# Performance work log

Measured on AMD Instinct MI355X. Metric: run time of the kernel, lower is better.

## Reference

```python
import jax, jax.numpy as jnp
from jax import lax
import numpy as np

NUM_HEADS = 4
EPS = 1e-5


def refl_conv(x, W, stride):
    # ReflectionPad2d(1) + Conv2d(k=3, bias=False), NCHW/OIHW
    x = jnp.pad(x, ((0, 0), (0, 0), (1, 1), (1, 1)), mode='reflect')
    return lax.conv_general_dilated(x, W, (stride, stride), 'VALID',
                                    dimension_numbers=('NCHW', 'OIHW', 'NCHW'))


def instance_norm(x):
    # nn.InstanceNorm2d (affine=False, biased var, eps=1e-5)
    m = jnp.mean(x, axis=(2, 3), keepdims=True)
    v = jnp.var(x, axis=(2, 3), keepdims=True)
    return (x - m) * lax.rsqrt(v + EPS)


def iln(x, rho, gamma, beta):
    # UGATIT Instance-Layer Norm; torch.var default is unbiased (ddof=1)
    in_m = jnp.mean(x, axis=(2, 3), keepdims=True)
    in_v = jnp.var(x, axis=(2, 3), keepdims=True, ddof=1)
    ln_m = jnp.mean(x, axis=(1, 2, 3), keepdims=True)
    ln_v = jnp.var(x, axis=(1, 2, 3), keepdims=True, ddof=1)
    out = rho * (x - in_m) * lax.rsqrt(in_v + EPS) \
        + (1.0 - rho) * (x - ln_m) * lax.rsqrt(ln_v + EPS)
    return out * gamma + beta


def upsample2(x):
    # nn.Upsample(scale_factor=2, mode='nearest')
    return jnp.repeat(jnp.repeat(x, 2, axis=2), 2, axis=3)


def pos_encoding(x):
    # sin/cos positional encoding over flattened HW, added per channel
    b, c, h, w = x.shape
    half = c // 2
    pos = jnp.arange(h * w, dtype=x.dtype)                  # [L]
    depths = jnp.arange(half, dtype=x.dtype) / half          # [c/2]
    rates = 1.0 / (10000.0 ** depths)
    ang = pos[:, None] * rates[None, :]                      # [L, c/2]
    pe = jnp.concatenate([jnp.sin(ang), jnp.cos(ang)], axis=-1)  # [L, c]
    return (x.reshape(b, c, h * w) + pe.T[None]).reshape(b, c, h, w)


def mha(q, k, v, num_heads):
    # q,k,v: [b, n, c]; hand-rolled QK^T-softmax-V (dropout=0)
    b, n, c = q.shape
    d = c // num_heads
    split = lambda t: t.reshape(b, t.shape[1], num_heads, d).transpose(0, 2, 1, 3)
    qh, kh, vh = split(q), split(k), split(v)                # [b, h, n, d]
    scores = jnp.einsum('bhid,bhjd->bhij', qh, kh) * (d ** -0.5)
    attn = jax.nn.softmax(scores, axis=-1)                   # full NxN materialized
    out = jnp.einsum('bhij,bhjd->bhid', attn, vh)
    return out.transpose(0, 2, 1, 3).reshape(b, n, c)


def setup_inputs() -> dict:
    key = jax.random.key(0)
    ks = jax.random.split(key, 8)
    W = 0.05
    return {
        'y': jax.random.normal(ks[0], (2, 256, 64, 64), jnp.float32),
        's': jax.random.normal(ks[1], (2, 128, 128, 128), jnp.float32),
        'w_blue_s': jax.random.normal(ks[2], (128, 128, 3, 3), jnp.float32) * W,
        'w_blue_y': jax.random.normal(ks[3], (128, 256, 3, 3), jnp.float32) * W,
        'w_purple': jax.random.normal(ks[4], (128, 128, 3, 3), jnp.float32) * W,
        'rho_p': jax.random.uniform(ks[5], (1, 128, 1, 1), jnp.float32),
        'gamma_p': jnp.ones((1, 128, 1, 1), jnp.float32),
        'beta_p': jnp.zeros((1, 128, 1, 1), jnp.float32),
        'w_green': jax.random.normal(ks[6], (128, 256, 3, 3), jnp.float32) * W,
        'rho_g': jax.random.uniform(ks[7], (1, 128, 1, 1), jnp.float32),
        'gamma_g': jnp.ones((1, 128, 1, 1), jnp.float32),
        'beta_g': jnp.zeros((1, 128, 1, 1), jnp.float32),
    }


def reference(y, s, w_blue_s, w_blue_y, w_purple, rho_p, gamma_p, beta_p,
              w_green, rho_g, gamma_g, beta_g):
    b, yc, yh, yw = y.shape
    sc = yc // 2
    # green_y: upsample -> refl conv -> ILN -> SiLU
    up_y = jax.nn.silu(iln(refl_conv(upsample2(y), w_green, 1), rho_g, gamma_g, beta_g))
    y_pe = pos_encoding(y)
    s_pe = pos_encoding(s)
    # blue_y (stride 1) -> q = k; blue_s (stride 2) -> v
    q2d = jax.nn.silu(instance_norm(refl_conv(y_pe, w_blue_y, 1)))   # [b, sc, yh, yw]
    v2d = jax.nn.silu(instance_norm(refl_conv(s_pe, w_blue_s, 2)))   # [b, sc, yh, yw]
    q = q2d.reshape(b, sc, yh * yw).transpose(0, 2, 1)               # [b, N, sc]
    v = v2d.reshape(b, sc, -1).transpose(0, 2, 1)
    out = mha(q, q, v, NUM_HEADS)                                     # [b, N, sc]
    mha2d = out.transpose(0, 2, 1).reshape(b, sc, yh, yw)
    # purple: upsample -> refl conv -> ILN -> sigmoid; gate s
    z = jax.nn.sigmoid(iln(refl_conv(upsample2(mha2d), w_purple, 1),
                           rho_p, gamma_p, beta_p)) * s
    return jnp.concatenate([z, up_y], axis=1)                         # [b, yc, 2yh, 2yw]
```

## Files before the change

kernel.cpp:

```cpp
#include <hip/hip_runtime.h>
#include <math.h>

#define EPS 1e-5f

typedef __attribute__((ext_vector_type(8))) _Float16 f16x8;
typedef __attribute__((ext_vector_type(4))) float f32x4;
typedef __attribute__((ext_vector_type(2))) __fp16 fp16x2;

union H8u { ushort4 u[2]; uint4 q; f16x8 h; };
union PKu { fp16x2 h; unsigned int u; };

__device__ __forceinline__ float sigmoidf_(float x){ return 1.f/(1.f+__expf(-x)); }

__device__ __forceinline__ unsigned short f2h(float f){
  union { _Float16 h; unsigned short u; } c;
  c.h = (_Float16)f;
  return c.u;
}

__device__ __forceinline__ void block_reduce2(float& s, float& s2){
  __shared__ float ls[16], ls2[16];
  #pragma unroll
  for (int off = 32; off; off >>= 1){
    s  += __shfl_down(s, off);
    s2 += __shfl_down(s2, off);
  }
  int wid = threadIdx.x >> 6, lane = threadIdx.x & 63;
  int nw = blockDim.x >> 6;
  if (lane == 0){ ls[wid] = s; ls2[wid] = s2; }
  __syncthreads();
  if (threadIdx.x == 0){
    float a = ls[0], b = ls2[0];
    for (int i = 1; i < nw; i++){ a += ls[i]; b += ls2[i]; }
    ls[0] = a; ls2[0] = b;
  }
  __syncthreads();
  s = ls[0]; s2 = ls2[0];
}

__device__ __forceinline__ unsigned short wffP_elem(const float* __restrict__ w, int Cin, int idx){
  int NCH = Cin >> 5;
  int per_tap = NCH << 9;
  int e = idx & 7, lane = (idx >> 3) & 63, chunk = (idx >> 9) % NCH;
  int tap = (idx / per_tap) % 9, coB = idx / (9 * per_tap);
  int lg = lane >> 4, lr = lane & 15;
  int co = coB * 16 + lr;
  int ch = chunk * 32 + ((e < 4) ? lg * 4 + e : 16 + lg * 4 + e - 4);
  return f2h(w[((long)co * Cin + ch) * 9 + tap]);
}

__device__ __forceinline__ unsigned short wffF_elem(const float* __restrict__ w, int Cin, int idx){
  int NCH = Cin >> 5;
  int per_tap = NCH << 9;
  int per_p = 8 * 4 * per_tap;
  int e = idx & 7, lane = (idx >> 3) & 63, chunk = (idx >> 9) % NCH;
  int tap = (idx / per_tap) % 4;
  int coB = (idx / (4 * per_tap)) % 8;
  int p = idx / per_p;
  int ph = p >> 1, pw = p & 1, kr = tap >> 1, kc = tap & 1;
  int lg = lane >> 4, lr = lane & 15;
  int co = coB * 16 + lr;
  int ch = chunk * 32 + ((e < 4) ? lg * 4 + e : 16 + lg * 4 + e - 4);
  const float* wb = &w[((long)co * Cin + ch) * 9];
  float sum = 0.f;
  for (int kh = 0; kh < 3; kh++){
    bool rok = (ph == 0) ? (kr == 0 ? kh == 0 : kh >= 1)
                         : (kr == 0 ? kh <= 1 : kh == 2);
    if (!rok) continue;
    for (int kw = 0; kw < 3; kw++){
      bool cok = (pw == 0) ? (kc == 0 ? kw == 0 : kw >= 1)
                           : (kc == 0 ? kw <= 1 : kw == 2);
      if (cok) sum += wb[kh * 3 + kw];
    }
  }
  return f2h(sum);
}

__global__ __launch_bounds__(256) void prep_all_kernel(
    const float* __restrict__ y, const float* __restrict__ s,
    unsigned short* __restrict__ y_peT, unsigned short* __restrict__ yT,
    unsigned short* __restrict__ s_peT,
    const float* __restrict__ wby, const float* __restrict__ wbs,
    const float* __restrict__ wg,  const float* __restrict__ wp,
    unsigned short* __restrict__ oby, unsigned short* __restrict__ obs,
    unsigned short* __restrict__ og,  unsigned short* __restrict__ op){
  __shared__ unsigned short tile[64][72];
  __shared__ unsigned short tile2[64][72];
  int bid = blockIdx.x;
  int tid = threadIdx.x;
  if (bid >= 1536){
    const int T0 = 294912, T1 = T0 + 147456, T2 = T1 + 524288, T3 = T2 + 262144;
    for (int idx = (bid - 1536) * 256 + tid; idx < T3; idx += 300 * 256){
      if (idx < T0)       oby[idx]      = wffP_elem(wby, 256, idx);
      else if (idx < T1)  obs[idx - T0] = wffP_elem(wbs, 128, idx - T0);
      else if (idx < T2)  og[idx - T1]  = wffF_elem(wg, 256, idx - T1);
      else                op[idx - T2]  = wffF_elem(wp, 128, idx - T2);
    }
    return;
  }
  const float* x; unsigned short *xt, *xt2;
  int C, L, half, bx, by, bz;
  if (bid < 512){
    x = y; xt = y_peT; xt2 = yT; C = 256; L = 4096; half = 128;
    bx = bid & 63; by = (bid >> 6) & 3; bz = bid >> 8;
  } else {
    int b2 = bid - 512;
    x = s; xt = s_peT; xt2 = nullptr; C = 128; L = 16384; half = 64;
    bx = b2 & 255; by = (b2 >> 8) & 1; bz = b2 >> 9;
  }
  int c0 = by * 64, l0 = bx * 64;
  int b = bz;
  const float l2r = 13.28771237954945f;
  #pragma unroll
  for (int i = 0; i < 4; i++){
    int id = tid + i * 256;
    int c = id >> 4, ch = (id & 15) * 4;
    int cg = c0 + c;
    float4 v = *(const float4*)&x[((long)b * C + cg) * L + l0 + ch];
    int d = cg < half ? cg : cg - half;
    float rate = exp2f(-l2r * (float)d / (float)half);
    float a0 = (float)(l0 + ch) * rate;
    float pe0, pe1, pe2, pe3;
    if (cg < half){ pe0 = sinf(a0); pe1 = sinf(a0 + rate); pe2 = sinf(a0 + 2.f*rate); pe3 = sinf(a0 + 3.f*rate); }
    else          { pe0 = cosf(a0); pe1 = cosf(a0 + rate); pe2 = cosf(a0 + 2.f*rate); pe3 = cosf(a0 + 3.f*rate); }
    ushort4 o;
    o.x = f2h(v.x + pe0); o.y = f2h(v.y + pe1);
    o.z = f2h(v.z + pe2); o.w = f2h(v.w + pe3);
    *(ushort4*)&tile[c][ch] = o;
    if (xt2){
      ushort4 o2;
      o2.x = f2h(v.x); o2.y = f2h(v.y); o2.z = f2h(v.z); o2.w = f2h(v.w);
      *(ushort4*)&tile2[c][ch] = o2;
    }
  }
  __syncthreads();
  #pragma unroll
  for (int i = 0; i < 2; i++){
    int id = tid + i * 256;
    int l = id >> 3, ch = (id & 7) * 8;
    ushort4 a, bq;
    a.x = tile[ch+0][l]; a.y = tile[ch+1][l]; a.z = tile[ch+2][l]; a.w = tile[ch+3][l];
    bq.x = tile[ch+4][l]; bq.y = tile[ch+5][l]; bq.z = tile[ch+6][l]; bq.w = tile[ch+7][l];
    unsigned short* opt = &xt[((long)b * L + l0 + l) * C + c0 + ch];
    *(ushort4*)opt = a;
    *(ushort4*)(opt + 4) = bq;
    if (xt2){
      ushort4 a2, b2;
      a2.x = tile2[ch+0][l]; a2.y = tile2[ch+1][l]; a2.z = tile2[ch+2][l]; a2.w = tile2[ch+3][l];
      b2.x = tile2[ch+4][l]; b2.y = tile2[ch+5][l]; b2.z = tile2[ch+6][l]; b2.w = tile2[ch+7][l];
      unsigned short* op2 = &xt2[((long)b * L + l0 + l) * C + c0 + ch];
      *(ushort4*)op2 = a2;
      *(ushort4*)(op2 + 4) = b2;
    }
  }
}

template<int NTAP, int CSHIFT, int UP, int STATS>
__device__ __forceinline__ void conv_body(
    const unsigned short* __restrict__ xt, const unsigned short* __restrict__ wff,
    unsigned short* __restrict__ out,
    float* __restrict__ psum, float* __restrict__ psq, int which,
    int Hin, int Win, int stride, int Wout, int woutLog, int HWout,
    int bz, char* stage, int* rowIdx){
  constexpr int Cin = 8 << CSHIFT;
  constexpr int NCHUNK = 1 << (CSHIFT - 2);
  int tid = threadIdx.x;
  int lane = tid & 63, wid = tid >> 6;
  int lg = lane >> 4, lr = lane & 15;
  int b, par = 0;
  if (UP){ par = bz & 3; b = bz >> 2; } else b = bz;
  const unsigned short* xb = xt + (long)b * Hin * Win * Cin;
  int coB = blockIdx.y * 4 + wid;

  if (UP){
    int ph = par >> 1, pw = par & 1;
    int ii = blockIdx.x;
    int VH = 2 * Hin, VW = 2 * Win;
    for (int id = tid; id < NTAP * 64; id += 256){
      int tap = id >> 6, r = id & 63;
      int kr = tap >> 1, kc = tap & 1;
      int v = 2 * ii + (ph == 0 ? (kr == 0 ? -1 : 0) : (kr == 0 ? 0 : 2));
      v = v < 0 ? -v : (v >= VH ? 2 * VH - 2 - v : v);
      int u = 2 * r + (pw == 0 ? (kc == 0 ? -1 : 0) : (kc == 0 ? 0 : 2));
      u = u < 0 ? -u : (u >= VW ? 2 * VW - 2 - u : u);
      rowIdx[tap * 64 + r] = (v >> 1) * Win + (u >> 1);
    }
  } else {
    int sp0 = blockIdx.x * 64;
    for (int id = tid; id < NTAP * 64; id += 256){
      int tap = id >> 6, r = id & 63;
      int kh = tap / 3, kw = tap - kh * 3;
      int sp = sp0 + r;
      int oh = sp >> woutLog, ow = sp & (Wout - 1);
      int ih = oh * stride - 1 + kh;
      ih = ih < 0 ? -ih : (ih >= Hin ? 2 * Hin - 2 - ih : ih);
      int iw = ow * stride - 1 + kw;
      iw = iw < 0 ? -iw : (iw >= Win ? 2 * Win - 2 - iw : iw);
      rowIdx[tap * 64 + r] = ih * Win + iw;
    }
  }

  f32x4 acc[4];
  #pragma unroll
  for (int f = 0; f < 4; f++) acc[f] = (f32x4){0.f, 0.f, 0.f, 0.f};

  const unsigned short* wbase =
      wff + ((long)((UP ? par : 0) * 8 + coB) * NTAP) * (NCHUNK * 512) + lane * 8;

  for (int tap = 0; tap < NTAP; tap++){
    __syncthreads();
    #pragma unroll
    for (int i2 = 0; i2 < NCHUNK; i2++){
      int id = tid + (i2 << 8);
      int sp = id >> CSHIFT;
      int c8 = (id & ((1 << CSHIFT) - 1)) << 3;
      int chunk = c8 >> 5, c = c8 & 31;
      int lgb = (c & 15) >> 2, hoff = (c >> 4) & 1;
      uint4 g = *(const uint4*)&xb[(long)rowIdx[tap * 64 + sp] * Cin + c8];
      int slot = ((chunk * 4 + (sp >> 4)) * 64 + lgb * 16 + (sp & 15)) * 16
                 + hoff * 8 + chunk * 16;
      *(uint2*)(stage + slot)       = make_uint2(g.x, g.y);
      *(uint2*)(stage + slot + 256) = make_uint2(g.z, g.w);
    }
    __syncthreads();
    const unsigned short* wp = wbase + (long)tap * (NCHUNK * 512);
    #pragma unroll
    for (int ch = 0; ch < NCHUNK; ch++){
      H8u A; A.q = *(const uint4*)(wp + ch * 512);
      #pragma unroll
      for (int f = 0; f < 4; f++){
        H8u X; X.q = *(const uint4*)(stage + ((ch * 4 + f) * 64 + lane) * 16 + ch * 16);
        acc[f] = __builtin_amdgcn_mfma_f32_16x16x32_f16(A.h, X.h, acc[f], 0, 0, 0);
      }
    }
  }

  unsigned short* ob = out + (long)b * 128 * HWout;
  #pragma unroll
  for (int f = 0; f < 4; f++){
    int spl = f * 16 + lr;
    long opos;
    if (UP){
      int oh = 2 * blockIdx.x + (par >> 1);
      int ow = 2 * spl + (par & 1);
      opos = (long)oh * Wout + ow;
    } else opos = (long)blockIdx.x * 64 + spl;
    #pragma unroll
    for (int r = 0; r < 4; r++){
      int co = coB * 16 + lg * 4 + r;
      ob[(long)co * HWout + opos] = f2h(acc[f][r]);
    }
  }

  if constexpr (STATS){
    float ts[4], tq[4];
    #pragma unroll
    for (int r = 0; r < 4; r++){ ts[r] = 0.f; tq[r] = 0.f; }
    #pragma unroll
    for (int f = 0; f < 4; f++)
      #pragma unroll
      for (int r = 0; r < 4; r++){
        float hv = (float)(_Float16)acc[f][r];
        ts[r] += hv; tq[r] += hv * hv;
      }
    #pragma unroll
    for (int off = 1; off < 16; off <<= 1){
      #pragma unroll
      for (int r = 0; r < 4; r++){
        ts[r] += __shfl_xor(ts[r], off);
        tq[r] += __shfl_xor(tq[r], off);
      }
    }
    if (lr == 0){
      int strip = blockIdx.x * 4 + par;
      #pragma unroll
      for (int r = 0; r < 4; r++){
        int co = coB * 16 + lg * 4 + r;
        long pidx = (((long)which * 2 + b) * 128 + co) * 256 + strip;
        psum[pidx] = ts[r];
        psq[pidx]  = tq[r];
      }
    }
  }
}

__global__ __launch_bounds__(256) void conv_blue_kernel(
    const unsigned short* __restrict__ y_peT, const unsigned short* __restrict__ s_peT,
    const unsigned short* __restrict__ wby, const unsigned short* __restrict__ wbs,
    unsigned short* __restrict__ qbuf, unsigned short* __restrict__ vbuf){
  __shared__ __align__(16) char stage[8 * 4112];
  __shared__ int rowIdx[9 * 64];
  int z = blockIdx.z;
  if (z < 2)
    conv_body<9,5,0,0>(y_peT, wby, qbuf, nullptr, nullptr, 0,
                       64, 64, 1, 64, 6, 4096, z, stage, rowIdx);
  else
    conv_body<9,4,0,0>(s_peT, wbs, vbuf, nullptr, nullptr, 0,
                       128, 128, 2, 64, 6, 4096, z - 2, stage, rowIdx);
}

__global__ __launch_bounds__(256) void conv_up_kernel(
    const unsigned short* __restrict__ yT, const unsigned short* __restrict__ mhaT,
    const unsigned short* __restrict__ wg, const unsigned short* __restrict__ wp,
    unsigned short* __restrict__ green_h, unsigned short* __restrict__ purple_h,
    float* __restrict__ psum, float* __restrict__ psq){
  __shared__ __align__(16) char stage[8 * 4112];
  __shared__ int rowIdx[4 * 64];
  int z = blockIdx.z;
  if (z < 8)
    conv_body<4,5,1,1>(yT, wg, green_h, psum, psq, 0,
                       64, 64, 1, 128, 7, 16384, z, stage, rowIdx);
  else
    conv_body<4,4,1,1>(mhaT, wp, purple_h, psum, psq, 1,
                       64, 64, 1, 128, 7, 16384, z - 8, stage, rowIdx);
}

__global__ __launch_bounds__(256) void in_silu2_kernel(
    const unsigned short* __restrict__ qx, unsigned short* __restrict__ outT,
    const unsigned short* __restrict__ vx, unsigned short* __restrict__ outV, int HW){
  int which = blockIdx.y;
  int bc = blockIdx.x;
  const unsigned short* p = (which ? vx : qx) + (long)bc * HW;
  int i0 = threadIdx.x * 16;
  H8u a, b2;
  a.q  = *(const uint4*)&p[i0];
  b2.q = *(const uint4*)&p[i0 + 8];
  float v[16];
  float s = 0.f, s2 = 0.f;
  #pragma unroll
  for (int j = 0; j < 8; j++){ v[j] = (float)a.h[j]; v[8+j] = (float)b2.h[j]; }
  #pragma unroll
  for (int j = 0; j < 16; j++){ s += v[j]; s2 += v[j]*v[j]; }
  block_reduce2(s, s2);
  float mean = s / (float)HW;
  float var  = s2 / (float)HW - mean * mean;
  float rstd = rsqrtf(var + EPS);
  if (which == 0){
    int b = bc >> 7, cg = bc & 127, h = cg >> 5, d = cg & 31;
    unsigned short* op = outT + ((long)(b * 4 + h) * HW) * 32 + d;
    #pragma unroll
    for (int j = 0; j < 16; j++){
      float t = (v[j] - mean) * rstd;
      t = t * sigmoidf_(t);
      op[(long)(i0 + j) * 32] = f2h(t);
    }
  } else {
    H8u o0, o1;
    #pragma unroll
    for (int j = 0; j < 8; j++){
      float t = (v[j] - mean) * rstd;
      o0.h[j] = (_Float16)(t * sigmoidf_(t));
      float t1 = (v[8+j] - mean) * rstd;
      o1.h[j] = (_Float16)(t1 * sigmoidf_(t1));
    }
    unsigned short* op = outV + (long)bc * HW + i0;
    *(uint4*)op = o0.q;
    *(uint4*)(op + 8) = o1.q;
  }
}

__global__ __launch_bounds__(1024, 8) void flash_attn_kernel(
    const unsigned short* __restrict__ qk,
    const unsigned short* __restrict__ vt,
    unsigned short* __restrict__ mhaT, int N){
  __shared__ float smem[16384];
  unsigned short* sstage = (unsigned short*)smem;
  const float SCALE2 = 0.25503257066404493f;

  int bh = blockIdx.y;
  int b = bh >> 2, h = bh & 3;
  int tid = threadIdx.x;
  int ks = tid >> 8;
  int t256 = tid & 255;
  int qg = (tid >> 6) & 3;
  int lane = tid & 63;
  int lg = lane >> 4, lr = lane & 15;
  const unsigned short* qbase = qk + (long)bh * N * 32;
  const unsigned short* vbase = vt + (long)(b * 128 + h * 32) * N;
  int ksu = ks * 4096;

  int q0w = blockIdx.x * 64 + qg * 16;
  f16x8 qf;
  {
    const unsigned short* qp = qbase + (long)(q0w + lr) * 32 + lg * 4;
    H8u Q;
    Q.u[0] = *(const ushort4*)qp;
    Q.u[1] = *(const ushort4*)(qp + 16);
    qf = Q.h;
    const _Float16 sc = (_Float16)SCALE2;
    #pragma unroll
    for (int j = 0; j < 8; j++) qf[j] = qf[j] * sc;
  }

  int skey = t256 >> 2, sq4 = t256 & 3;
  int kdst = ksu + (((skey >> 4) * 4 + (sq4 & 1) * 2) * 16 + (skey & 15)) * 8 + (sq4 >> 1) * 4;
  int sd = t256 >> 3, soct = t256 & 7;
  int vx = (soct >> 2) * 2 + (soct & 1);
  int vdst = ksu + 2048 +
      ((((soct >> 2) * 2 + (sd >> 4)) * 4 + (soct & 1) * 2) * 16 + ((sd & 15) ^ vx)) * 8 +
      ((soct >> 1) & 1) * 4;

  float m_run = -1e30f, l_run = 0.f;
  f32x4 acc0 = {0.f,0.f,0.f,0.f}, acc1 = {0.f,0.f,0.f,0.f};

  const int NT = N >> 8;

  {
    int k0 = ks * NT * 64;
    uint4 kl = *(const uint4*)(qbase + (long)(k0 + skey) * 32 + sq4 * 8);
    *(uint2*)(&sstage[kdst])       = make_uint2(kl.x, kl.y);
    *(uint2*)(&sstage[kdst + 128]) = make_uint2(kl.z, kl.w);
    uint4 vl = *(const uint4*)(vbase + (long)sd * N + k0 + soct * 8);
    *(uint2*)(&sstage[vdst])       = make_uint2(vl.x, vl.y);
    *(uint2*)(&sstage[vdst + 128]) = make_uint2(vl.z, vl.w);
  }
  __syncthreads();

  for (int t = 0; t < NT; t++){
    int bufc = (t & 1) << 14;
    int bufn = ((t + 1) & 1) << 14;
    uint4 kl, vl;
    bool have_next = (t + 1 < NT);
    if (have_next){
      int k0n = (ks * NT + t + 1) * 64;
      kl = *(const uint4*)(qbase + (long)(k0n + skey) * 32 + sq4 * 8);
      vl = *(const uint4*)(vbase + (long)sd * N + k0n + soct * 8);
    }

    f32x4 st[4];
    #pragma unroll
    for (int kb = 0; kb < 4; kb++){
      H8u K;
      K.q = *(const uint4*)(&sstage[bufc + ksu + (kb * 64 + lane) * 8]);
      st[kb] = __builtin_amdgcn_mfma_f32_16x16x32_f16(K.h, qf,
                  (f32x4){0.f,0.f,0.f,0.f}, 0, 0, 0);
    }

    float mk0 = fmaxf(fmaxf(fmaxf(st[0][0], st[0][1]), st[0][2]), st[0][3]);
    float mk1 = fmaxf(fmaxf(fmaxf(st[1][0], st[1][1]), st[1][2]), st[1][3]);
    float mk2 = fmaxf(fmaxf(fmaxf(st[2][0], st[2][1]), st[2][2]), st[2][3]);
    float mk3 = fmaxf(fmaxf(fmaxf(st[3][0], st[3][1]), st[3][2]), st[3][3]);
    float mt = fmaxf(fmaxf(fmaxf(mk0, mk1), mk2), mk3);
    mt = fmaxf(mt, __shfl_xor(mt, 16));
    mt = fmaxf(mt, __shfl_xor(mt, 32));

    bool noresc = __all(mt <= m_run + 8.f);
    float m_new = noresc ? m_run : fmaxf(m_run, mt);

    float lt = 0.f;
    unsigned int pup[8];
    #pragma unroll
    for (int kb = 0; kb < 4; kb++)
      #pragma unroll
      for (int rp = 0; rp < 2; rp++){
        float p0 = __builtin_amdgcn_exp2f(st[kb][2*rp]   - m_new);
        float p1 = __builtin_amdgcn_exp2f(st[kb][2*rp+1] - m_new);
        lt += p0 + p1;
        PKu pk;
        pk.h = __builtin_amdgcn_cvt_pkrtz(p0, p1);
        pup[kb * 2 + rp] = pk.u;
      }
    lt += __shfl_xor(lt, 16);
    lt += __shfl_xor(lt, 32);

    if (noresc){
      l_run += lt;
    } else {
      float fscale = __builtin_amdgcn_exp2f(m_run - m_new);
      l_run = l_run * fscale + lt;
      float fr[4];
      #pragma unroll
      for (int r = 0; r < 4; r++) fr[r] = __shfl(fscale, lg * 4 + r);
      #pragma unroll
      for (int r = 0; r < 4; r++){ acc0[r] *= fr[r]; acc1[r] *= fr[r]; }
      m_run = m_new;
    }

    #pragma unroll
    for (int m = 0; m < 2; m++){
      int xr = m * 2 + (lg >> 1);
      int laneV = lg * 16 + (lr ^ xr);
      H8u P, V0, V1;
      P.q = make_uint4(pup[4*m], pup[4*m+1], pup[4*m+2], pup[4*m+3]);
      V0.q = *(const uint4*)(&sstage[bufc + ksu + 2048 + ((m * 2 + 0) * 64 + laneV) * 8]);
      V1.q = *(const uint4*)(&sstage[bufc + ksu + 2048 + ((m * 2 + 1) * 64 + laneV) * 8]);
      acc0 = __builtin_amdgcn_mfma_f32_16x16x32_f16(P.h, V0.h, acc0, 0, 0, 0);
      acc1 = __builtin_amdgcn_mfma_f32_16x16x32_f16(P.h, V1.h, acc1, 0, 0, 0);
    }

    if (have_next){
      *(uint2*)(&sstage[bufn + kdst])       = make_uint2(kl.x, kl.y);
      *(uint2*)(&sstage[bufn + kdst + 128]) = make_uint2(kl.z, kl.w);
      *(uint2*)(&sstage[bufn + vdst])       = make_uint2(vl.x, vl.y);
      *(uint2*)(&sstage[bufn + vdst + 128]) = make_uint2(vl.z, vl.w);
    }
    __syncthreads();
  }

  float* accM = smem;
  float* mM   = smem + 8448;
  float* lM   = smem + 8704;
  #pragma unroll
  for (int r = 0; r < 4; r++){
    accM[((qg * 4 + ks) * 16 + (lg * 4 + r)) * 33 + lr]      = acc0[r];
    accM[((qg * 4 + ks) * 16 + (lg * 4 + r)) * 33 + 16 + lr] = acc1[r];
  }
  if (lg == 0){
    mM[(qg * 4 + ks) * 16 + lr] = m_run;
    lM[(qg * 4 + ks) * 16 + lr] = l_run;
  }
  __syncthreads();
  if (ks == 0){
    int q = lane >> 2, dc = lane & 3;
    float ms[4], es[4];
    float m = -1e30f;
    #pragma unroll
    for (int s = 0; s < 4; s++){ ms[s] = mM[(qg * 4 + s) * 16 + q]; m = fmaxf(m, ms[s]); }
    float l = 0.f;
    #pragma unroll
    for (int s = 0; s < 4; s++){
      es[s] = __builtin_amdgcn_exp2f(ms[s] - m);
      l += lM[(qg * 4 + s) * 16 + q] * es[s];
    }
    float inv = 1.f / l;
    float o[8];
    #pragma unroll
    for (int j = 0; j < 8; j++) o[j] = 0.f;
    #pragma unroll
    for (int s = 0; s < 4; s++){
      const float* ap = &accM[((qg * 4 + s) * 16 + q) * 33 + dc * 8];
      #pragma unroll
      for (int j = 0; j < 8; j++) o[j] += ap[j] * es[s];
    }
    ushort4 o0, o1;
    o0.x = f2h(o[0]*inv); o0.y = f2h(o[1]*inv); o0.z = f2h(o[2]*inv); o0.w = f2h(o[3]*inv);
    o1.x = f2h(o[4]*inv); o1.y = f2h(o[5]*inv); o1.z = f2h(o[6]*inv); o1.w = f2h(o[7]*inv);
    unsigned short* op = &mhaT[((long)b * N + q0w + q) * 128 + h * 32 + dc * 8];
    *(ushort4*)op = o0;
    *(ushort4*)(op + 4) = o1;
  }
}

__global__ __launch_bounds__(64) void stats3_kernel(
    const float* __restrict__ psum, const float* __restrict__ psq,
    float* __restrict__ statsbase){
  int blockch = blockIdx.x;
  int which = blockch >> 8, bc = blockch & 255;
  const float* ps = psum + (long)blockch * 256;
  const float* pq = psq  + (long)blockch * 256;
  float s = 0.f, s2 = 0.f;
  for (int i = threadIdx.x; i < 256; i += 64){ s += ps[i]; s2 += pq[i]; }
  #pragma unroll
  for (int off = 32; off; off >>= 1){
    s  += __shfl_down(s, off);
    s2 += __shfl_down(s2, off);
  }
  if (threadIdx.x == 0){
    float* sums = statsbase + which * 512;
    sums[bc] = s;
    sums[256 + bc] = s2;
  }
}

__global__ __launch_bounds__(256) void iln_finalize2_kernel(
    const unsigned short* __restrict__ xg, const unsigned short* __restrict__ xp,
    const float* __restrict__ statsbase,
    const float* __restrict__ rho_p, const float* __restrict__ gamma_p,
    const float* __restrict__ beta_p,
    const float* __restrict__ rho_g, const float* __restrict__ gamma_g,
    const float* __restrict__ beta_g,
    const float* __restrict__ gate,
    float* __restrict__ out,
    int HW, int C){
  int zp = blockIdx.z;
  int bc = blockIdx.y;
  int b = bc / C, c = bc % C;
  const float* sums   = statsbase + (zp ? 0 : 512);
  const float* sumsqs = sums + 256;

  float s = 0.f, s2 = 0.f;
  if (threadIdx.x < 128){
    int cc = b * C + threadIdx.x;
    s = sums[cc]; s2 = sumsqs[cc];
  }
  block_reduce2(s, s2);
  float lsum = s, lsumsq = s2;

  float n = (float)HW;
  float im = sums[bc] / n;
  float iv = (sumsqs[bc] / n - im * im) * (n / (n - 1.f));
  float ir = rsqrtf(iv + EPS);
  float n2 = n * (float)C;
  float lm = lsum / n2;
  float lv = (lsumsq / n2 - lm * lm) * (n2 / (n2 - 1.f));
  float lr = rsqrtf(lv + EPS);
  float r  = zp ? rho_g[c]   : rho_p[c];
  float g  = zp ? gamma_g[c] : gamma_p[c];
  float bb = zp ? beta_g[c]  : beta_p[c];

  const unsigned short* xp_ = (zp ? xg : xp) + (long)bc * HW;
  const float* gp = zp ? nullptr : (gate + (long)bc * HW);
  float* op = out + ((long)(b * 256 + (zp ? 128 : 0) + c)) * HW;
  int i0 = (blockIdx.x * 256 + threadIdx.x) * 8;
  H8u a; a.q = *(const uint4*)&xp_[i0];
  float4 o0, o1;
  float res[8];
  #pragma unroll
  for (int j = 0; j < 8; j++){
    float xv = (float)a.h[j];
    float t = r * (xv - im) * ir + (1.f - r) * (xv - lm) * lr;
    t = t * g + bb;
    float sg = sigmoidf_(t);
    res[j] = zp ? t * sg : sg;
  }
  if (!zp){
    float4 g0 = *(const float4*)&gp[i0];
    float4 g1 = *(const float4*)&gp[i0 + 4];
    res[0] *= g0.x; res[1] *= g0.y; res[2] *= g0.z; res[3] *= g0.w;
    res[4] *= g1.x; res[5] *= g1.y; res[6] *= g1.z; res[7] *= g1.w;
  }
  o0.x = res[0]; o0.y = res[1]; o0.z = res[2]; o0.w = res[3];
  o1.x = res[4]; o1.y = res[5]; o1.z = res[6]; o1.w = res[7];
  *(float4*)&op[i0] = o0;
  *(float4*)&op[i0 + 4] = o1;
}

extern "C" void kernel_launch(void* const* d_in, const int* in_sizes, int n_in,
                              void* d_out, int out_size, void* d_ws, size_t ws_size,
                              hipStream_t stream){
  const float* y        = (const float*)d_in[0];
  const float* s        = (const float*)d_in[1];
  const float* w_blue_s = (const float*)d_in[2];
  const float* w_blue_y = (const float*)d_in[3];
  const float* w_purple = (const float*)d_in[4];
  const float* rho_p    = (const float*)d_in[5];
  const float* gamma_p  = (const float*)d_in[6];
  const float* beta_p   = (const float*)d_in[7];
  const float* w_green  = (const float*)d_in[8];
  const float* rho_g    = (const float*)d_in[9];
  const float* gamma_g  = (const float*)d_in[10];
  const float* beta_g   = (const float*)d_in[11];
  float* out = (float*)d_out;
  float* ws  = (float*)d_ws;

  const int B = 2, SC = 128, N = 4096, NS = 16384;

  unsigned short* s_peT = (unsigned short*)ws;
  unsigned short* y_peT = (unsigned short*)(ws + 2097152);
  unsigned short* yT    = (unsigned short*)(ws + 3145728);
  unsigned short* purple_h = (unsigned short*)ws;
  unsigned short* qbuf_h = (unsigned short*)(ws + 4194304);
  unsigned short* vbuf_h = (unsigned short*)(ws + 4718592);
  unsigned short* mhaT   = (unsigned short*)(ws + 5242880);
  unsigned short* qk_bf  = (unsigned short*)(ws + 5767168);
  unsigned short* v_bf   = (unsigned short*)(ws + 6291456);
  unsigned short* green_h = (unsigned short*)(ws + 6815744);
  unsigned short* wffP_blues = (unsigned short*)(ws + 8912896);
  unsigned short* wffP_bluey = (unsigned short*)(ws + 8986624);
  unsigned short* wffF_green = (unsigned short*)(ws + 9134080);
  unsigned short* wffF_purple = (unsigned short*)(ws + 9396224);
  float* stats = ws + 9527296;
  float* psum  = ws + 9528320;
  float* psq   = ws + 9659392;

  dim3 blk(256);

  prep_all_kernel<<<dim3(1836), blk, 0, stream>>>(
      y, s, y_peT, yT, s_peT,
      w_blue_y, w_blue_s, w_green, w_purple,
      wffP_bluey, wffP_blues, wffF_green, wffF_purple);

  conv_blue_kernel<<<dim3(64, 2, 4), blk, 0, stream>>>(
      y_peT, s_peT, wffP_bluey, wffP_blues, qbuf_h, vbuf_h);

  in_silu2_kernel<<<dim3(B * SC, 2), blk, 0, stream>>>(qbuf_h, qk_bf, vbuf_h, v_bf, N);

  flash_attn_kernel<<<dim3(N / 64, B * 4), dim3(1024), 0, stream>>>(qk_bf, v_bf, mhaT, N);

  conv_up_kernel<<<dim3(64, 2, 16), blk, 0, stream>>>(
      yT, mhaT, wffF_green, wffF_purple, green_h, purple_h, psum, psq);

  stats3_kernel<<<dim3(512), dim3(64), 0, stream>>>(psum, psq, stats);

  iln_finalize2_kernel<<<dim3(8, B * SC, 2), blk, 0, stream>>>(
      green_h, purple_h, stats,
      rho_p, gamma_p, beta_p, rho_g, gamma_g, beta_g,
      s, out, NS, SC);
}
```

Measured before the change: 127.9 us.

## Fuse instance-norm statistics into blue conv epilogue and tile the q transpose

The blue convolutions now write per-strip partial sums and sums of squares in their epilogue. A new qkv_transform kernel reads these partials instead of re-reducing the full planes, and transposes q through a shared-memory tile so its global writes are coalesced rather than strided 2-byte stores. The flash-attention kernel also moves the cross-lane reduction of the row sum out of the inner loop to a single reduction at the end. In exchange the conv epilogue does extra work, the partial-stat buffers use more workspace, and the instance-norm stats are now computed from fp16-rounded values in a different order.

```diff
diff --git a/kernel.cpp b/kernel.cpp
--- a/kernel.cpp
+++ b/kernel.cpp
@@ -9,6 +9,7 @@
 
 union H8u { ushort4 u[2]; uint4 q; f16x8 h; };
 union PKu { fp16x2 h; unsigned int u; };
+union U8u { unsigned short us[8]; uint4 q; };
 
 __device__ __forceinline__ float sigmoidf_(float x){ return 1.f/(1.f+__expf(-x)); }
 
@@ -164,6 +165,7 @@
     int bz, char* stage, int* rowIdx){
   constexpr int Cin = 8 << CSHIFT;
   constexpr int NCHUNK = 1 << (CSHIFT - 2);
+  constexpr int PSTRIDE = UP ? 256 : 64;
   int tid = threadIdx.x;
   int lane = tid & 63, wid = tid >> 6;
   int lg = lane >> 4, lr = lane & 15;
@@ -272,11 +274,11 @@
       }
     }
     if (lr == 0){
-      int strip = blockIdx.x * 4 + par;
+      int strip = UP ? (blockIdx.x * 4 + par) : blockIdx.x;
       #pragma unroll
       for (int r = 0; r < 4; r++){
         int co = coB * 16 + lg * 4 + r;
-        long pidx = (((long)which * 2 + b) * 128 + co) * 256 + strip;
+        long pidx = (((long)which * 2 + b) * 128 + co) * PSTRIDE + strip;
         psum[pidx] = ts[r];
         psq[pidx]  = tq[r];
       }
@@ -287,15 +289,16 @@
 __global__ __launch_bounds__(256) void conv_blue_kernel(
     const unsigned short* __restrict__ y_peT, const unsigned short* __restrict__ s_peT,
     const unsigned short* __restrict__ wby, const unsigned short* __restrict__ wbs,
-    unsigned short* __restrict__ qbuf, unsigned short* __restrict__ vbuf){
+    unsigned short* __restrict__ qbuf, unsigned short* __restrict__ vbuf,
+    float* __restrict__ psumB, float* __restrict__ psqB){
   __shared__ __align__(16) char stage[8 * 4112];
   __shared__ int rowIdx[9 * 64];
   int z = blockIdx.z;
   if (z < 2)
-    conv_body<9,5,0,0>(y_peT, wby, qbuf, nullptr, nullptr, 0,
+    conv_body<9,5,0,1>(y_peT, wby, qbuf, psumB, psqB, 0,
                        64, 64, 1, 64, 6, 4096, z, stage, rowIdx);
   else
-    conv_body<9,4,0,0>(s_peT, wbs, vbuf, nullptr, nullptr, 0,
+    conv_body<9,4,0,1>(s_peT, wbs, vbuf, psumB, psqB, 1,
                        128, 128, 2, 64, 6, 4096, z - 2, stage, rowIdx);
 }
 
@@ -315,47 +318,78 @@
                        64, 64, 1, 128, 7, 16384, z - 8, stage, rowIdx);
 }
 
-__global__ __launch_bounds__(256) void in_silu2_kernel(
-    const unsigned short* __restrict__ qx, unsigned short* __restrict__ outT,
-    const unsigned short* __restrict__ vx, unsigned short* __restrict__ outV, int HW){
-  int which = blockIdx.y;
-  int bc = blockIdx.x;
-  const unsigned short* p = (which ? vx : qx) + (long)bc * HW;
-  int i0 = threadIdx.x * 16;
-  H8u a, b2;
-  a.q  = *(const uint4*)&p[i0];
-  b2.q = *(const uint4*)&p[i0 + 8];
-  float v[16];
-  float s = 0.f, s2 = 0.f;
-  #pragma unroll
-  for (int j = 0; j < 8; j++){ v[j] = (float)a.h[j]; v[8+j] = (float)b2.h[j]; }
-  #pragma unroll
-  for (int j = 0; j < 16; j++){ s += v[j]; s2 += v[j]*v[j]; }
-  block_reduce2(s, s2);
-  float mean = s / (float)HW;
-  float var  = s2 / (float)HW - mean * mean;
-  float rstd = rsqrtf(var + EPS);
-  if (which == 0){
-    int b = bc >> 7, cg = bc & 127, h = cg >> 5, d = cg & 31;
-    unsigned short* op = outT + ((long)(b * 4 + h) * HW) * 32 + d;
-    #pragma unroll
-    for (int j = 0; j < 16; j++){
-      float t = (v[j] - mean) * rstd;
-      t = t * sigmoidf_(t);
-      op[(long)(i0 + j) * 32] = f2h(t);
-    }
+__global__ __launch_bounds__(256) void qkv_transform_kernel(
+    const unsigned short* __restrict__ qbuf, const unsigned short* __restrict__ vbuf,
+    const float* __restrict__ psumB, const float* __restrict__ psqB,
+    unsigned short* __restrict__ outT, unsigned short* __restrict__ outV){
+  int bid = blockIdx.x;
+  int tid = threadIdx.x;
+  if (bid < 256){
+    __shared__ unsigned short tile[32][137];
+    __shared__ float sm[32], sr[32];
+    int pt = bid & 31, h = (bid >> 5) & 3, bb = bid >> 7;
+    int c_local = tid >> 3, i0 = tid & 7;
+    int cg = h * 32 + c_local;
+    long base = ((long)bb * 128 + cg) * 64;
+    float s = 0.f, s2 = 0.f;
+    #pragma unroll
+    for (int k = 0; k < 8; k++){
+      s  += psumB[base + i0 + k * 8];
+      s2 += psqB[base + i0 + k * 8];
+    }
+    #pragma unroll
+    for (int off = 1; off < 8; off <<= 1){
+      s  += __shfl_xor(s, off);
+      s2 += __shfl_xor(s2, off);
+    }
+    if (i0 == 0){
+      float mean = s * (1.f / 4096.f);
+      float var  = s2 * (1.f / 4096.f) - mean * mean;
+      sm[c_local] = mean;
+      sr[c_local] = rsqrtf(var + EPS);
+    }
+    __syncthreads();
+    float mean = sm[c_local], rstd = sr[c_local];
+    const unsigned short* qp = qbuf + ((long)bb * 128 + cg) * 4096 + pt * 128 + i0 * 16;
+    H8u a, b2;
+    a.q  = *(const uint4*)qp;
+    b2.q = *(const uint4*)(qp + 8);
+    #pragma unroll
+    for (int j = 0; j < 8; j++){
+      float t0 = ((float)a.h[j] - mean) * rstd;
+      tile[c_local][i0 * 16 + j] = f2h(t0 * sigmoidf_(t0));
+      float t1 = ((float)b2.h[j] - mean) * rstd;
+      tile[c_local][i0 * 16 + 8 + j] = f2h(t1 * sigmoidf_(t1));
+    }
+    __syncthreads();
+    int pos = tid >> 1, halfd = tid & 1;
+    U8u w0, w1;
+    #pragma unroll
+    for (int k = 0; k < 8; k++) w0.us[k] = tile[halfd * 16 + k][pos];
+    #pragma unroll
+    for (int k = 0; k < 8; k++) w1.us[k] = tile[halfd * 16 + 8 + k][pos];
+    unsigned short* op = outT + ((long)((bb * 4 + h) * 4096 + pt * 128 + pos)) * 32 + halfd * 16;
+    *(uint4*)op = w0.q;
+    *(uint4*)(op + 8) = w1.q;
   } else {
-    H8u o0, o1;
+    int vb = bid - 256;
+    int bc = vb >> 1;
+    long gbase = ((long)(2 + (bc >> 7)) * 128 + (bc & 127)) * 64;
+    float s = 0.f, s2 = 0.f;
+    if (tid < 64){ s = psumB[gbase + tid]; s2 = psqB[gbase + tid]; }
+    block_reduce2(s, s2);
+    float mean = s * (1.f / 4096.f);
+    float var  = s2 * (1.f / 4096.f) - mean * mean;
+    float rstd = rsqrtf(var + EPS);
+    long e0 = (long)vb * 2048 + tid * 8;
+    H8u a; a.q = *(const uint4*)&vbuf[e0];
+    H8u o;
     #pragma unroll
     for (int j = 0; j < 8; j++){
-      float t = (v[j] - mean) * rstd;
-      o0.h[j] = (_Float16)(t * sigmoidf_(t));
-      float t1 = (v[8+j] - mean) * rstd;
-      o1.h[j] = (_Float16)(t1 * sigmoidf_(t1));
-    }
-    unsigned short* op = outV + (long)bc * HW + i0;
-    *(uint4*)op = o0.q;
-    *(uint4*)(op + 8) = o1.q;
+      float t = ((float)a.h[j] - mean) * rstd;
+      o.h[j] = (_Float16)(t * sigmoidf_(t));
+    }
+    *(uint4*)&outV[e0] = o.q;
   }
 }
 
@@ -460,8 +494,6 @@
         pk.h = __builtin_amdgcn_cvt_pkrtz(p0, p1);
         pup[kb * 2 + rp] = pk.u;
       }
-    lt += __shfl_xor(lt, 16);
-    lt += __shfl_xor(lt, 32);
 
     if (noresc){
       l_run += lt;
@@ -496,6 +528,9 @@
     }
     __syncthreads();
   }
+
+  l_run += __shfl_xor(l_run, 16);
+  l_run += __shfl_xor(l_run, 32);
 
   float* accM = smem;
   float* mM   = smem + 8448;
@@ -662,6 +697,8 @@
   float* stats = ws + 9527296;
   float* psum  = ws + 9528320;
   float* psq   = ws + 9659392;
+  float* psumB = ws + 9790464;
+  float* psqB  = ws + 9823232;
 
   dim3 blk(256);
 
@@ -671,9 +708,10 @@
       wffP_bluey, wffP_blues, wffF_green, wffF_purple);
 
   conv_blue_kernel<<<dim3(64, 2, 4), blk, 0, stream>>>(
-      y_peT, s_peT, wffP_bluey, wffP_blues, qbuf_h, vbuf_h);
-
-  in_silu2_kernel<<<dim3(B * SC, 2), blk, 0, stream>>>(qbuf_h, qk_bf, vbuf_h, v_bf, N);
+      y_peT, s_peT, wffP_bluey, wffP_blues, qbuf_h, vbuf_h, psumB, psqB);
+
+  qkv_transform_kernel<<<dim3(768), blk, 0, stream>>>(
+      qbuf_h, vbuf_h, psumB, psqB, qk_bf, v_bf);
 
   flash_attn_kernel<<<dim3(N / 64, B * 4), dim3(1024), 0, stream>>>(qk_bf, v_bf, mhaT, N);
 
```

New measurement: 140.1 us. 9.6% more time.
